# Kernel optimization log

Hardware: AMD Instinct MI355X
Metric: run time of the kernel (lower is better)

Reference implementation:

```python
import jax, jax.numpy as jnp
import numpy as np

INPUT_DIM = 2048
EMBED_DIM = 128


def setup_inputs() -> dict:
    key = jax.random.key(0)
    kx, kw, kb, kv = jax.random.split(key, 4)
    x = jax.random.normal(kx, (16384, INPUT_DIM), dtype=jnp.float32)
    # nn.Linear(input_dim, 1): weight [1, D] (init std=0.01), bias [1]
    W = jax.random.normal(kw, (1, INPUT_DIM), dtype=jnp.float32) * 0.01
    b = jax.random.normal(kb, (1,), dtype=jnp.float32) * 0.01
    # nn.Embedding(input_dim, embedding_dim): V [D, K] (init std=0.01)
    V = jax.random.normal(kv, (INPUT_DIM, EMBED_DIM), dtype=jnp.float32) * 0.01
    return {"x": x, "W": W, "b": b, "V": V}


def reference(x, W, b, V):
    # linear part: x @ W^T + b -> [B, 1]
    linear_part = x @ W.T + b
    # FM 2nd-order interaction via the standard identity:
    # 0.5 * sum_k ( (sum_d x_d V_dk)^2 - sum_d x_d^2 V_dk^2 )
    # equals the original sum_square - square_sum over weighted embeddings.
    xv = x @ V                       # [B, K]
    x2v2 = (x * x) @ (V * V)         # [B, K]
    interaction = 0.5 * jnp.sum(xv * xv - x2v2, axis=1, keepdims=True)
    return linear_part + interaction
```

## Files before the change

kernel.cpp:

```cpp
#include <hip/hip_runtime.h>
#include <hip/hip_bf16.h>

#define K_DIM 2048
#define N_DIM 128
#define BM 64
#define BK 64
#define NTILES (K_DIM / BK)
#define VT_CHUNK 16384

typedef __bf16 bf16x8 __attribute__((ext_vector_type(8)));
typedef float f32x4 __attribute__((ext_vector_type(4)));

__device__ __forceinline__ float dot4(f32x4 a, f32x4 b) {
    return a.x * b.x + a.y * b.y + a.z * b.z + a.w * b.w;
}

__device__ __forceinline__ void gload16(const void* g, void* lds) {
    __builtin_amdgcn_global_load_lds(
        (const __attribute__((address_space(1))) unsigned int*)g,
        (__attribute__((address_space(3))) unsigned int*)lds,
        16, 0, 0);
}

__global__ __launch_bounds__(256) void fm_prep(const float* __restrict__ V,
                                               char* __restrict__ VtS,
                                               float* __restrict__ s) {
    __shared__ float tile[64][132];
    const int t = threadIdx.x;
    const int kb = blockIdx.x;
    const int k0 = kb * 64;
#pragma unroll
    for (int i = 0; i < 8; ++i) {
        int idx = i * 256 + t;
        int kk = idx >> 5;
        int nq = (idx & 31) * 4;
        *(f32x4*)&tile[kk][nq] = *(const f32x4*)(V + (size_t)(k0 + kk) * N_DIM + nq);
    }
    __syncthreads();
    {
        const int n = t >> 1;
        const int half = t & 1;
        const int sw = (n & 7) << 4;
        char* dstbase = VtS + (size_t)kb * VT_CHUNK + n * 128;
#pragma unroll
        for (int g = 0; g < 4; ++g) {
            int kkg = half * 32 + g * 8;
            bf16x8 o;
#pragma unroll
            for (int e = 0; e < 8; ++e) o[e] = (__bf16)tile[kkg + e][n];
            *(bf16x8*)(dstbase + ((kkg * 2) ^ sw)) = o;
        }
    }
    if (t < 64) {
        float a = 0.f;
#pragma unroll
        for (int nq = 0; nq < 32; ++nq) {
            f32x4 v = *(f32x4*)&tile[t][nq * 4];
            a += dot4(v, v);
        }
        s[k0 + t] = a;
    }
}

__global__ __launch_bounds__(512, 2) void fm_main(const float* __restrict__ x,
                                                  const float* __restrict__ W,
                                                  const float* __restrict__ bptr,
                                                  const char* __restrict__ VtS,
                                                  const float* __restrict__ s,
                                                  float* __restrict__ out) {
    __shared__ __align__(16) char xbuf[2][16384];
    __shared__ __align__(16) char vbuf[2][16384];
    __shared__ __align__(16) float Wl[2048];
    __shared__ __align__(16) float Sl[2048];
    __shared__ float lin_lds[4][16];
    __shared__ float sq_lds[4][16];
    __shared__ float ss_lds[4][2][16];

    const int tid = threadIdx.x;
    const int w = tid >> 6;
    const int l = tid & 63;
    const int lr = l & 15;
    const int lg = l >> 4;
    const int wr = w >> 1;
    const int wc = w & 1;
    const int row0 = blockIdx.x * BM;

    *(f32x4*)&Wl[tid * 4] = *(const f32x4*)(W + tid * 4);
    *(f32x4*)&Sl[tid * 4] = *(const f32x4*)(s + tid * 4);

    const bool isX = (w < 4);
    const char* src[4];
    int loff[4];
    if (isX) {
#pragma unroll
        for (int j = 0; j < 4; ++j) {
            int gi = w * 4 + j;
            int rowt = gi * 4 + lg;
            int koff = (lr * 16) ^ ((rowt & 7) << 4);
            src[j] = (const char*)x + (size_t)(row0 + rowt) * (K_DIM * 4) + koff;
            loff[j] = gi * 1024;
        }
    } else {
#pragma unroll
        for (int j = 0; j < 4; ++j) {
            int vi = (w - 4) * 4 + j;
            src[j] = VtS + vi * 1024 + l * 16;
            loff[j] = vi * 1024;
        }
    }

    f32x4 acc[4];
#pragma unroll
    for (int c = 0; c < 4; ++c) acc[c] = (f32x4){0.f, 0.f, 0.f, 0.f};
    float lin = 0.f, sq = 0.f;

    if (isX) {
#pragma unroll
        for (int j = 0; j < 4; ++j) gload16(src[j], &xbuf[0][loff[j]]);
    } else {
#pragma unroll
        for (int j = 0; j < 4; ++j) gload16(src[j], &vbuf[0][loff[j]]);
    }
    __syncthreads();

    const int rowt = wr * 16 + lr;
    const int swA = (rowt & 7) << 4;
    const char* arowbase = &xbuf[0][0] + rowt * 256;

    for (int t = 0; t < NTILES; ++t) {
        const int cur = t & 1;
        if (t < NTILES - 1) {
            if (isX) {
#pragma unroll
                for (int j = 0; j < 4; ++j)
                    gload16(src[j] + (size_t)(t + 1) * (BK * 4), &xbuf[cur ^ 1][loff[j]]);
            } else {
#pragma unroll
                for (int j = 0; j < 4; ++j)
                    gload16(src[j] + (size_t)(t + 1) * VT_CHUNK, &vbuf[cur ^ 1][loff[j]]);
            }
        }

        const char* arow = &xbuf[cur][0] + rowt * 256;
        const char* vb = &vbuf[cur][0];

        bf16x8 af[2];
        f32x4 alo[2], ahi[2];
#pragma unroll
        for (int kb = 0; kb < 2; ++kb) {
            const int kA = kb * 128 + lg * 32;
            alo[kb] = *(const f32x4*)(arow + (kA ^ swA));
            ahi[kb] = *(const f32x4*)(arow + ((kA + 16) ^ swA));
            af[kb][0] = (__bf16)alo[kb].x; af[kb][1] = (__bf16)alo[kb].y;
            af[kb][2] = (__bf16)alo[kb].z; af[kb][3] = (__bf16)alo[kb].w;
            af[kb][4] = (__bf16)ahi[kb].x; af[kb][5] = (__bf16)ahi[kb].y;
            af[kb][6] = (__bf16)ahi[kb].z; af[kb][7] = (__bf16)ahi[kb].w;
        }
        if (wc == 0) {
            const int ki = t * 64 + lg * 8;
#pragma unroll
            for (int kb = 0; kb < 2; ++kb) {
                f32x4 w0 = *(const f32x4*)&Wl[ki + kb * 32];
                f32x4 w1 = *(const f32x4*)&Wl[ki + kb * 32 + 4];
                f32x4 s0 = *(const f32x4*)&Sl[ki + kb * 32];
                f32x4 s1 = *(const f32x4*)&Sl[ki + kb * 32 + 4];
                lin += dot4(alo[kb], w0) + dot4(ahi[kb], w1);
                sq  += dot4(alo[kb] * alo[kb], s0) + dot4(ahi[kb] * ahi[kb], s1);
            }
        }
#pragma unroll
        for (int c = 0; c < 4; ++c) {
            const int nt = wc * 64 + c * 16 + lr;
            const int swB = (nt & 7) << 4;
            const char* brow = vb + nt * 128;
#pragma unroll
            for (int kb = 0; kb < 2; ++kb) {
                bf16x8 bf = *(const bf16x8*)(brow + ((kb * 64 + lg * 16) ^ swB));
                acc[c] = __builtin_amdgcn_mfma_f32_16x16x32_bf16(af[kb], bf, acc[c], 0, 0, 0);
            }
        }
        __syncthreads();
    }
    (void)arowbase;

    f32x4 vss = (f32x4){0.f, 0.f, 0.f, 0.f};
#pragma unroll
    for (int c = 0; c < 4; ++c) vss += acc[c] * acc[c];
#pragma unroll
    for (int m = 1; m < 16; m <<= 1) {
        vss.x += __shfl_xor(vss.x, m);
        vss.y += __shfl_xor(vss.y, m);
        vss.z += __shfl_xor(vss.z, m);
        vss.w += __shfl_xor(vss.w, m);
    }
    if (lr == 0) {
        ss_lds[wr][wc][lg * 4 + 0] = vss.x;
        ss_lds[wr][wc][lg * 4 + 1] = vss.y;
        ss_lds[wr][wc][lg * 4 + 2] = vss.z;
        ss_lds[wr][wc][lg * 4 + 3] = vss.w;
    }
    if (wc == 0) {
        lin += __shfl_xor(lin, 16); lin += __shfl_xor(lin, 32);
        sq  += __shfl_xor(sq, 16);  sq  += __shfl_xor(sq, 32);
        if (l < 16) { lin_lds[wr][l] = lin; sq_lds[wr][l] = sq; }
    }
    __syncthreads();
    if (tid < 64) {
        const int wrI = tid >> 4, r16 = tid & 15;
        out[row0 + tid] = lin_lds[wrI][r16] + bptr[0]
            + 0.5f * (ss_lds[wrI][0][r16] + ss_lds[wrI][1][r16] - sq_lds[wrI][r16]);
    }
}

extern "C" void kernel_launch(void* const* d_in, const int* in_sizes, int n_in,
                              void* d_out, int out_size, void* d_ws, size_t ws_size,
                              hipStream_t stream) {
    const float* x = (const float*)d_in[0];
    const float* W = (const float*)d_in[1];
    const float* b = (const float*)d_in[2];
    const float* V = (const float*)d_in[3];
    float* out = (float*)d_out;

    char* VtS = (char*)d_ws;
    float* s = (float*)((char*)d_ws + 32 * VT_CHUNK);

    fm_prep<<<32, 256, 0, stream>>>(V, VtS, s);
    fm_main<<<256, 512, 0, stream>>>(x, W, b, VtS, s, out);
}
```

Before: 204.8 us.

## Triple-buffer x tiles with non-temporal loads and explicit waitcnt barriers

The x stream gets a third LDS buffer and is prefetched two tiles ahead, while V stays double-buffered. Its loads use a non-temporal cache hint, since x is read only once. The generic __syncthreads is replaced by explicit s_waitcnt vmcnt plus s_barrier, so waves keep later loads in flight and wait only for the tile they need. LDS use per block rises by 16KB, which can cut occupancy with two 512-thread blocks per CU, and the wait-count logic is fragile if load counts change.

Measured after the change: 203.5 us. Within noise of the previous version (-0.6%).

```diff
diff --git a/kernel.cpp b/kernel.cpp
--- a/kernel.cpp
+++ b/kernel.cpp
@@ -20,6 +20,12 @@
         (const __attribute__((address_space(1))) unsigned int*)g,
         (__attribute__((address_space(3))) unsigned int*)lds,
         16, 0, 0);
+}
+__device__ __forceinline__ void gload16_nt(const void* g, void* lds) {
+    __builtin_amdgcn_global_load_lds(
+        (const __attribute__((address_space(1))) unsigned int*)g,
+        (__attribute__((address_space(3))) unsigned int*)lds,
+        16, 0, 2);
 }
 
 __global__ __launch_bounds__(256) void fm_prep(const float* __restrict__ V,
@@ -68,7 +74,7 @@
                                                   const char* __restrict__ VtS,
                                                   const float* __restrict__ s,
                                                   float* __restrict__ out) {
-    __shared__ __align__(16) char xbuf[2][16384];
+    __shared__ __align__(16) char xbuf[3][16384];
     __shared__ __align__(16) char vbuf[2][16384];
     __shared__ __align__(16) float Wl[2048];
     __shared__ __align__(16) float Sl[2048];
@@ -116,33 +122,39 @@
 
     if (isX) {
 #pragma unroll
-        for (int j = 0; j < 4; ++j) gload16(src[j], &xbuf[0][loff[j]]);
+        for (int j = 0; j < 4; ++j) gload16_nt(src[j], &xbuf[0][loff[j]]);
+#pragma unroll
+        for (int j = 0; j < 4; ++j) gload16_nt(src[j] + 256, &xbuf[1][loff[j]]);
+        asm volatile("s_waitcnt vmcnt(4) lgkmcnt(0)" ::: "memory");
     } else {
 #pragma unroll
         for (int j = 0; j < 4; ++j) gload16(src[j], &vbuf[0][loff[j]]);
-    }
-    __syncthreads();
+        asm volatile("s_waitcnt vmcnt(0) lgkmcnt(0)" ::: "memory");
+    }
+    __builtin_amdgcn_s_barrier();
+    __builtin_amdgcn_sched_barrier(0);
 
     const int rowt = wr * 16 + lr;
     const int swA = (rowt & 7) << 4;
-    const char* arowbase = &xbuf[0][0] + rowt * 256;
-
+
+    int xr = 0, xi = 2, vr = 0;
     for (int t = 0; t < NTILES; ++t) {
-        const int cur = t & 1;
-        if (t < NTILES - 1) {
-            if (isX) {
+        if (isX) {
+            if (t + 2 < NTILES) {
 #pragma unroll
                 for (int j = 0; j < 4; ++j)
-                    gload16(src[j] + (size_t)(t + 1) * (BK * 4), &xbuf[cur ^ 1][loff[j]]);
-            } else {
+                    gload16_nt(src[j] + (size_t)(t + 2) * (BK * 4), &xbuf[xi][loff[j]]);
+            }
+        } else {
+            if (t + 1 < NTILES) {
 #pragma unroll
                 for (int j = 0; j < 4; ++j)
-                    gload16(src[j] + (size_t)(t + 1) * VT_CHUNK, &vbuf[cur ^ 1][loff[j]]);
-            }
-        }
-
-        const char* arow = &xbuf[cur][0] + rowt * 256;
-        const char* vb = &vbuf[cur][0];
+                    gload16(src[j] + (size_t)(t + 1) * VT_CHUNK, &vbuf[vr ^ 1][loff[j]]);
+            }
+        }
+
+        const char* arow = &xbuf[xr][0] + rowt * 256;
+        const char* vb = &vbuf[vr][0];
 
         bf16x8 af[2];
         f32x4 alo[2], ahi[2];
@@ -179,9 +191,23 @@
                 acc[c] = __builtin_amdgcn_mfma_f32_16x16x32_bf16(af[kb], bf, acc[c], 0, 0, 0);
             }
         }
-        __syncthreads();
-    }
-    (void)arowbase;
+
+        if (t < NTILES - 1) {
+            if (isX) {
+                if (t + 2 < NTILES)
+                    asm volatile("s_waitcnt vmcnt(4)" ::: "memory");
+                else
+                    asm volatile("s_waitcnt vmcnt(0)" ::: "memory");
+            } else {
+                asm volatile("s_waitcnt vmcnt(0)" ::: "memory");
+            }
+            __builtin_amdgcn_s_barrier();
+            __builtin_amdgcn_sched_barrier(0);
+        }
+        xr = (xr == 2) ? 0 : xr + 1;
+        xi = (xi == 2) ? 0 : xi + 1;
+        vr ^= 1;
+    }
 
     f32x4 vss = (f32x4){0.f, 0.f, 0.f, 0.f};
 #pragma unroll
@@ -205,10 +231,11 @@
         if (l < 16) { lin_lds[wr][l] = lin; sq_lds[wr][l] = sq; }
     }
     __syncthreads();
-    if (tid < 64) {
+    if (tid < BM) {
         const int wrI = tid >> 4, r16 = tid & 15;
         out[row0 + tid] = lin_lds[wrI][r16] + bptr[0]
-            + 0.5f * (ss_lds[wrI][0][r16] + ss_lds[wrI][1][r16] - sq_lds[wrI][r16]);
+            + 0.5f * (ss_lds[wrI][0][r16] + ss_lds[wrI][1][r16]
+                      - sq_lds[wrI][r16]);
     }
 }
 
```
